# Kernel tuning notes

Hardware: AMD Instinct MI355X
Metric: run time of the kernel (lower is better)

Reference implementation:

```python
import jax, jax.numpy as jnp
import numpy as np


def _rank_transform_ascending(flat):
    # torch: _, idx = sort(flat, descending=False); flat[idx] = linspace(0,1,n)+1/n
    n = flat.shape[0]
    order = jnp.argsort(flat)  # ascending
    prob = jnp.linspace(0.0, 1.0, n, dtype=flat.dtype) + jnp.asarray(1.0 / n, flat.dtype)
    return jnp.zeros_like(flat).at[order].set(prob)


def corr_attention(query, key, value):
    # score[b,h,i,j] = cosine-like similarity q_i . k_j / (|q_i| |k_j|)
    score = jnp.einsum('bhid,bhjd->bhij', query, key)
    q_len = jnp.sqrt(jnp.sum(query * query, axis=-1, keepdims=True)) + 1e-5  # [b,h,s,1]
    k_len = jnp.sqrt(jnp.sum(key * key, axis=-1, keepdims=True)) + 1e-5      # [b,h,s,1]
    score = score / (q_len * jnp.swapaxes(k_len, -1, -2))
    signal = jnp.sign(score)
    size = score.shape
    flat = jnp.abs(score).reshape(-1)
    ranked = _rank_transform_ascending(flat)
    score = -jnp.log(ranked).reshape(size) * signal
    score = score / jnp.sum(jnp.abs(score), axis=-1, keepdims=True)
    return jnp.einsum('bhij,bhjd->bhid', score, value)


def setup_inputs() -> dict:
    key0 = jax.random.key(0)
    kq, kk, kv = jax.random.split(key0, 3)
    B, H, S, D = 4, 8, 1024, 64
    query = jax.random.normal(kq, (B, H, S, D), dtype=jnp.float32)
    key = jax.random.normal(kk, (B, H, S, D), dtype=jnp.float32)
    value = jax.random.normal(kv, (B, H, S, D), dtype=jnp.float32)
    return {"query": query, "key": key, "value": value}


def reference(query, key, value):
    # Attention.forward with mode='season'
    return corr_attention(query, key, value)
```

## Files before the change

kernel.cpp:

```cpp
#include <hip/hip_runtime.h>
#include <math.h>
#include <stdint.h>

#define S_LEN 1024
#define D_DIM 64
#define BH    32
#define KSHIFT 13
#define NBINS 130048u
#define HOT_LO 115712u
#define NHOT   14336u
#define HIST_LO 117760u
#define NHOT_H  12288u
#define NCHUNK 254
#define HBLK   256
#define INV_NM1 (1.0f/33554431.0f)
#define INV_N   (2.9802322387695312e-08f)
#define FIX_TH  1e-4f

typedef _Float16 half8 __attribute__((ext_vector_type(8)));
typedef short    short8 __attribute__((ext_vector_type(8)));
typedef float    floatx4 __attribute__((ext_vector_type(4)));

__global__ __launch_bounds__(256) void norms_kernel(
    const float* __restrict__ Q, const float* __restrict__ K,
    double* __restrict__ qinvD, double* __restrict__ kinvD,
    float* __restrict__ qinvF, float* __restrict__ kinvF) {
  int row  = blockIdx.x * 4 + (threadIdx.x >> 6);
  int lane = threadIdx.x & 63;
  const float* src; double* dstD; float* dstF; int r = row;
  if (row < BH * S_LEN) { src = Q; dstD = qinvD; dstF = qinvF; }
  else                  { src = K; dstD = kinvD; dstF = kinvF; r = row - BH * S_LEN; }
  double v = (double)src[(size_t)r * D_DIM + lane];
  double s = v * v;
  #pragma unroll
  for (int off = 32; off; off >>= 1) s += __shfl_down(s, off);
  if (lane == 0) {
    double inv = 1.0 / (sqrt(s) + 1e-5);
    dstD[r] = inv;
    dstF[r] = (float)inv;
  }
}

__device__ __forceinline__ void bf16_split(float x, short& hi, short& lo) {
  unsigned u = __float_as_uint(x);
  unsigned h = (u + 0x7FFFu + ((u >> 16) & 1u)) >> 16;
  float hf = __uint_as_float(h << 16);
  float lf = x - hf;
  hi = (short)h;
  lo = (short)(__float_as_uint(lf) >> 16);
}

__global__ __launch_bounds__(256) void qk_mfma_kernel(
    const float* __restrict__ Q, const float* __restrict__ K,
    const float* __restrict__ qinvF, const float* __restrict__ kinvF,
    float* __restrict__ score) {
  __shared__ short Qhi[64][72], Qlo[64][72];
  __shared__ short Khi[64][72], Klo[64][72];
  int bh = blockIdx.z;
  int i0 = blockIdx.y * 64;
  int j0 = blockIdx.x * 64;
  int tid = threadIdx.x;
  const float* Qb = Q + ((size_t)bh * S_LEN + i0) * D_DIM;
  const float* Kb = K + ((size_t)bh * S_LEN + j0) * D_DIM;
  #pragma unroll
  for (int l = 0; l < 4; ++l) {
    int idx4 = l * 256 + tid;
    int row  = idx4 >> 4;
    int c4   = idx4 & 15;
    float qi = qinvF[(size_t)bh * S_LEN + i0 + row];
    float4 v = ((const float4*)Qb)[idx4];
    float qv[4] = {v.x * qi, v.y * qi, v.z * qi, v.w * qi};
    short qh[4], ql[4];
    #pragma unroll
    for (int c = 0; c < 4; ++c) bf16_split(qv[c], qh[c], ql[c]);
    *(short4*)&Qhi[row][c4 * 4] = make_short4(qh[0], qh[1], qh[2], qh[3]);
    *(short4*)&Qlo[row][c4 * 4] = make_short4(ql[0], ql[1], ql[2], ql[3]);
    float kj = kinvF[(size_t)bh * S_LEN + j0 + row];
    float4 w = ((const float4*)Kb)[idx4];
    float kv[4] = {w.x * kj, w.y * kj, w.z * kj, w.w * kj};
    short kh[4], kl[4];
    #pragma unroll
    for (int c = 0; c < 4; ++c) bf16_split(kv[c], kh[c], kl[c]);
    *(short4*)&Khi[row][c4 * 4] = make_short4(kh[0], kh[1], kh[2], kh[3]);
    *(short4*)&Klo[row][c4 * 4] = make_short4(kl[0], kl[1], kl[2], kl[3]);
  }
  __syncthreads();
  int wave = tid >> 6;
  int lane = tid & 63;
  int m    = lane & 15;
  int quad = lane >> 4;
  floatx4 acc[4];
  #pragma unroll
  for (int n = 0; n < 4; ++n) acc[n] = (floatx4){0.f, 0.f, 0.f, 0.f};
  #pragma unroll
  for (int ks = 0; ks < 2; ++ks) {
    int kb = ks * 32 + quad * 8;
    short8 a_hi = *(const short8*)&Qhi[wave * 16 + m][kb];
    short8 a_lo = *(const short8*)&Qlo[wave * 16 + m][kb];
    #pragma unroll
    for (int nt = 0; nt < 4; ++nt) {
      short8 b_hi = *(const short8*)&Khi[nt * 16 + m][kb];
      short8 b_lo = *(const short8*)&Klo[nt * 16 + m][kb];
      acc[nt] = __builtin_amdgcn_mfma_f32_16x16x32_bf16(a_hi, b_hi, acc[nt], 0, 0, 0);
      acc[nt] = __builtin_amdgcn_mfma_f32_16x16x32_bf16(a_hi, b_lo, acc[nt], 0, 0, 0);
      acc[nt] = __builtin_amdgcn_mfma_f32_16x16x32_bf16(a_lo, b_hi, acc[nt], 0, 0, 0);
    }
  }
  #pragma unroll
  for (int r = 0; r < 4; ++r) {
    float* op = score + ((size_t)bh * S_LEN + i0 + wave * 16 + quad * 4 + r) * S_LEN + j0 + m;
    #pragma unroll
    for (int nt = 0; nt < 4; ++nt)
      op[nt * 16] = acc[nt][r];
  }
}

__global__ __launch_bounds__(1024) void hist_kernel(
    float* __restrict__ score, const float* __restrict__ Q, const float* __restrict__ K,
    const double* __restrict__ qinvD, const double* __restrict__ kinvD,
    unsigned* __restrict__ hist, unsigned char* __restrict__ partial) {
  __shared__ unsigned lh[NHOT_H];
  int tid = threadIdx.x;
  int lane = tid & 63;
  for (unsigned i = tid; i < NHOT_H; i += 1024) lh[i] = 0u;
  __syncthreads();
  const float4* p = (const float4*)score + (size_t)blockIdx.x * 32768;
  #pragma unroll 2
  for (int it = 0; it < 32; ++it) {
    float4 v = p[it * 1024 + tid];
    float vv[4] = {v.x, v.y, v.z, v.w};
    bool anyf = (fabsf(vv[0]) < FIX_TH) | (fabsf(vv[1]) < FIX_TH) |
                (fabsf(vv[2]) < FIX_TH) | (fabsf(vv[3]) < FIX_TH);
    unsigned long long am = __ballot(anyf);
    while (am) {
      int src = (int)(__ffsll((long long)am) - 1);
      am &= am - 1;
      unsigned base4 = (unsigned)(blockIdx.x * 32768u + (unsigned)(it * 1024 + tid));
      unsigned b4 = __shfl(base4, src);
      #pragma unroll
      for (int c = 0; c < 4; ++c) {
        float sc = __shfl(vv[c], src);
        if (fabsf(sc) < FIX_TH) {
          unsigned flat = b4 * 4u + (unsigned)c;
          unsigned bh = flat >> 20, i = (flat >> 10) & 1023u, j = flat & 1023u;
          double qd = (double)Q[((size_t)bh * S_LEN + i) * D_DIM + lane];
          double kd = (double)K[((size_t)bh * S_LEN + j) * D_DIM + lane];
          double pd = qd * kd;
          #pragma unroll
          for (int off = 32; off; off >>= 1) pd += __shfl_down(pd, off);
          float corr = 0.f;
          if (lane == 0)
            corr = (float)(pd * qinvD[(size_t)bh * S_LEN + i] * kinvD[(size_t)bh * S_LEN + j]);
          corr = __shfl(corr, 0);
          if (lane == src) {
            vv[c] = corr;
            score[(size_t)flat] = corr;
          }
        }
      }
    }
    #pragma unroll
    for (int c = 0; c < 4; ++c) {
      unsigned b = __float_as_uint(fabsf(vv[c])) >> KSHIFT;
      if (b >= NBINS) b = NBINS - 1u;
      if (b >= HIST_LO) atomicAdd(&lh[b - HIST_LO], 1u);
      else              atomicAdd(&hist[b], 1u);
    }
  }
  __syncthreads();
  unsigned char* dst = partial + (size_t)blockIdx.x * NHOT_H;
  for (unsigned i = tid; i < NHOT_H; i += 1024) dst[i] = (unsigned char)lh[i];
}

__global__ __launch_bounds__(256) void hreduce_kernel(
    const unsigned char* __restrict__ partial, unsigned* __restrict__ hist) {
  unsigned bin = blockIdx.x * 256 + threadIdx.x;
  unsigned s = 0;
  #pragma unroll 8
  for (int b = 0; b < HBLK; ++b) s += (unsigned)partial[(size_t)b * NHOT_H + bin];
  hist[HIST_LO + bin] = s;
}

__global__ __launch_bounds__(256) void vt_kernel(
    const float* __restrict__ V, _Float16* __restrict__ Vt) {
  __shared__ _Float16 T[64][72];
  int bh = blockIdx.y, j0 = blockIdx.x * 64, tid = threadIdx.x;
  const float* Vb = V + ((size_t)bh * S_LEN + j0) * D_DIM;
  #pragma unroll
  for (int l = 0; l < 4; ++l) {
    int idx = l * 256 + tid;
    int jr = idx >> 4, d4 = idx & 15;
    float4 v = ((const float4*)Vb)[idx];
    T[d4*4+0][jr] = (_Float16)v.x;
    T[d4*4+1][jr] = (_Float16)v.y;
    T[d4*4+2][jr] = (_Float16)v.z;
    T[d4*4+3][jr] = (_Float16)v.w;
  }
  __syncthreads();
  _Float16* Ob = Vt + (size_t)bh * D_DIM * S_LEN + j0;
  #pragma unroll
  for (int l = 0; l < 2; ++l) {
    int idx = l * 256 + tid;
    int d = idx >> 3, jc = idx & 7;
    uint4 val = *(const uint4*)&T[d][jc*8];
    *(uint4*)(Ob + (size_t)d * S_LEN + jc*8) = val;
  }
}

__global__ __launch_bounds__(256) void scan1_kernel(const unsigned* __restrict__ hist,
                                                    unsigned* __restrict__ csum) {
  __shared__ unsigned sd[256];
  int c = blockIdx.x, t = threadIdx.x;
  const unsigned* p = hist + (size_t)c * 512;
  sd[t] = p[t] + p[t + 256];
  __syncthreads();
  for (int off = 128; off; off >>= 1) {
    if (t < off) sd[t] += sd[t + off];
    __syncthreads();
  }
  if (t == 0) csum[c] = sd[0];
}

__global__ __launch_bounds__(256) void scan2_kernel(unsigned* __restrict__ csum) {
  __shared__ unsigned d[256];
  int t = threadIdx.x;
  unsigned v = (t < NCHUNK) ? csum[t] : 0u;
  d[t] = v; __syncthreads();
  for (int off = 1; off < 256; off <<= 1) {
    unsigned x = (t >= off) ? d[t - off] : 0u;
    __syncthreads();
    d[t] += x;
    __syncthreads();
  }
  if (t < NCHUNK) csum[t] = d[t] - v;
}

__global__ __launch_bounds__(256) void scan3_kernel(const unsigned* __restrict__ hist,
                                                    const unsigned* __restrict__ csum,
                                                    _Float16* __restrict__ tTab16) {
  __shared__ unsigned ts[256];
  int c = blockIdx.x, t = threadIdx.x;
  const unsigned* p = hist + (size_t)c * 512 + t * 2;
  unsigned l0 = p[0], l1 = p[1];
  unsigned s = l0 + l1;
  ts[t] = s; __syncthreads();
  for (int off = 1; off < 256; off <<= 1) {
    unsigned x = (t >= off) ? ts[t - off] : 0u;
    __syncthreads();
    ts[t] += x;
    __syncthreads();
  }
  unsigned base = csum[c] + ts[t] - s;
  int idx = c * 512 + t * 2;
  float r0 = (float)base + 0.5f * ((float)l0 - 1.0f);
  tTab16[idx]     = (_Float16)(-__logf(fmaf(r0, INV_NM1, INV_N)));
  float r1 = (float)(base + l0) + 0.5f * ((float)l1 - 1.0f);
  tTab16[idx + 1] = (_Float16)(-__logf(fmaf(r1, INV_NM1, INV_N)));
}

__global__ __launch_bounds__(256) void pv_mfma_kernel(
    const float* __restrict__ score, const _Float16* __restrict__ Vt,
    const unsigned short* __restrict__ tTab16, float* __restrict__ out) {
  __shared__ unsigned short ldsT[NHOT];
  int tid = threadIdx.x;
  {
    const unsigned* gsrc = (const unsigned*)(tTab16 + HOT_LO);
    unsigned* ldst = (unsigned*)ldsT;
    #pragma unroll
    for (int i = 0; i < 28; ++i)
      ldst[i * 256 + tid] = gsrc[i * 256 + tid];
  }
  __syncthreads();

  int bh   = blockIdx.y;
  int wave = tid >> 6;
  int lane = tid & 63;
  int m    = lane & 15;
  int quad = lane >> 4;
  int i0   = blockIdx.x * 64 + wave * 16;
  const float*    Sb = score + ((size_t)bh * S_LEN + i0 + m) * S_LEN;
  const _Float16* Vb = Vt + (size_t)bh * D_DIM * S_LEN;
  floatx4 acc[4];
  #pragma unroll
  for (int n = 0; n < 4; ++n) acc[n] = (floatx4){0.f, 0.f, 0.f, 0.f};
  float rsum = 0.f;

  for (int ks = 0; ks < 32; ++ks) {
    int k0 = ks * 32 + quad * 8;
    float4 s0 = *(const float4*)(Sb + k0);
    float4 s1 = *(const float4*)(Sb + k0 + 4);
    float sv[8] = {s0.x, s0.y, s0.z, s0.w, s1.x, s1.y, s1.z, s1.w};
    union { unsigned short u[8]; half8 h; } af;
    #pragma unroll
    for (int e = 0; e < 8; ++e) {
      unsigned u = __float_as_uint(sv[e]);
      unsigned a = u & 0x7fffffffu;
      unsigned b = a >> KSHIFT;
      if (b > NBINS - 1u) b = NBINS - 1u;
      unsigned short tb;
      if (b >= HOT_LO) tb = ldsT[b - HOT_LO];
      else             tb = tTab16[b];
      if (a == 0u) tb = 0;
      af.u[e] = (unsigned short)(tb ^ ((u >> 16) & 0x8000u));
      unsigned short tabs = (unsigned short)(tb & 0x7fffu);
      _Float16 th = __builtin_bit_cast(_Float16, tabs);
      rsum += (float)th;
    }
    half8 bf[4];
    #pragma unroll
    for (int n = 0; n < 4; ++n)
      bf[n] = *(const half8*)(Vb + (size_t)(n * 16 + m) * S_LEN + k0);
    #pragma unroll
    for (int n = 0; n < 4; ++n)
      acc[n] = __builtin_amdgcn_mfma_f32_16x16x32_f16(af.h, bf[n], acc[n], 0, 0, 0);
  }

  rsum += __shfl_xor(rsum, 16);
  rsum += __shfl_xor(rsum, 32);
  float inv = 1.0f / rsum;
  #pragma unroll
  for (int r = 0; r < 4; ++r) {
    int row = quad * 4 + r;
    float invr = __shfl(inv, row);
    float* op = out + ((size_t)bh * S_LEN + i0 + row) * D_DIM + m;
    #pragma unroll
    for (int n = 0; n < 4; ++n)
      op[n * 16] = acc[n][r] * invr;
  }
}

extern "C" void kernel_launch(void* const* d_in, const int* in_sizes, int n_in,
                              void* d_out, int out_size, void* d_ws, size_t ws_size,
                              hipStream_t stream) {
  const float* Q = (const float*)d_in[0];
  const float* K = (const float*)d_in[1];
  const float* V = (const float*)d_in[2];
  float* out = (float*)d_out;
  char* ws = (char*)d_ws;
  float*         score   = (float*)(ws);
  unsigned*      hist    = (unsigned*)(ws + 134217728);
  unsigned char* partial = (unsigned char*)(ws + 134737920);
  double*        qinvD   = (double*)(ws + 137883648);
  double*        kinvD   = (double*)(ws + 138145792);
  float*         qinvF   = (float*)(ws + 138407936);
  float*         kinvF   = (float*)(ws + 138539008);
  _Float16*      Vt      = (_Float16*)(ws + 134737920);
  unsigned*      csum    = (unsigned*)(ws + 139194368);
  _Float16*      tTab16  = (_Float16*)(ws + 139195392);

  hipMemsetAsync(hist, 0, NBINS * sizeof(unsigned), stream);
  norms_kernel<<<(2 * BH * S_LEN) / 4, 256, 0, stream>>>(Q, K, qinvD, kinvD, qinvF, kinvF);
  qk_mfma_kernel<<<dim3(16, 16, BH), 256, 0, stream>>>(Q, K, qinvF, kinvF, score);
  hist_kernel<<<HBLK, 1024, 0, stream>>>(score, Q, K, qinvD, kinvD, hist, partial);
  hreduce_kernel<<<NHOT_H / 256, 256, 0, stream>>>(partial, hist);
  vt_kernel<<<dim3(16, BH), 256, 0, stream>>>(V, Vt);
  scan1_kernel<<<NCHUNK, 256, 0, stream>>>(hist, csum);
  scan2_kernel<<<1, 256, 0, stream>>>(csum);
  scan3_kernel<<<NCHUNK, 256, 0, stream>>>(hist, csum, tTab16);
  pv_mfma_kernel<<<dim3(16, BH), 256, 0, stream>>>(
      score, Vt, (const unsigned short*)tTab16, out);
}
```

Baseline: 218.0 us.

## Split PV reduction across waves with LDS atomics and shrink hot table

The PV kernel now gives each block 16 rows, with its four waves each covering a quarter of the key dimension. Partial MFMA accumulators and row sums are combined through LDS atomics, and the result is written as float4 stores. The grid grows from 512 to 2048 blocks to raise occupancy and memory-level parallelism on the large score read. The LDS table preload shrinks to the NHOT_H range, which cuts preload cost per block but sends more lookups to global memory. Each block still preloads the table, so more blocks means more total preload traffic, and the LDS atomics add overhead.

Measured after the change: 238.8 us. +9.5%, slower.

```diff
diff --git a/kernel.cpp b/kernel.cpp
--- a/kernel.cpp
+++ b/kernel.cpp
@@ -7,8 +7,6 @@
 #define BH    32
 #define KSHIFT 13
 #define NBINS 130048u
-#define HOT_LO 115712u
-#define NHOT   14336u
 #define HIST_LO 117760u
 #define NHOT_H  12288u
 #define NCHUNK 254
@@ -261,14 +259,22 @@
 __global__ __launch_bounds__(256) void pv_mfma_kernel(
     const float* __restrict__ score, const _Float16* __restrict__ Vt,
     const unsigned short* __restrict__ tTab16, float* __restrict__ out) {
-  __shared__ unsigned short ldsT[NHOT];
+  __shared__ unsigned short ldsT[NHOT_H];
+  __shared__ float accS[16][72];
+  __shared__ float rsumS[16];
   int tid = threadIdx.x;
   {
-    const unsigned* gsrc = (const unsigned*)(tTab16 + HOT_LO);
+    const unsigned* gsrc = (const unsigned*)(tTab16 + HIST_LO);
     unsigned* ldst = (unsigned*)ldsT;
     #pragma unroll
-    for (int i = 0; i < 28; ++i)
+    for (int i = 0; i < 24; ++i)
       ldst[i * 256 + tid] = gsrc[i * 256 + tid];
+  }
+  if (tid < 16) rsumS[tid] = 0.f;
+  {
+    int r = tid >> 4, c = tid & 15;
+    #pragma unroll
+    for (int cc = 0; cc < 4; ++cc) accS[r][c * 4 + cc] = 0.f;
   }
   __syncthreads();
 
@@ -277,15 +283,16 @@
   int lane = tid & 63;
   int m    = lane & 15;
   int quad = lane >> 4;
-  int i0   = blockIdx.x * 64 + wave * 16;
-  const float*    Sb = score + ((size_t)bh * S_LEN + i0 + m) * S_LEN;
-  const _Float16* Vb = Vt + (size_t)bh * D_DIM * S_LEN;
+  int i0   = blockIdx.x * 16;
+  const float*    Sb = score + ((size_t)bh * S_LEN + i0 + m) * S_LEN + wave * 256;
+  const _Float16* Vb = Vt + (size_t)bh * D_DIM * S_LEN + wave * 256;
   floatx4 acc[4];
   #pragma unroll
   for (int n = 0; n < 4; ++n) acc[n] = (floatx4){0.f, 0.f, 0.f, 0.f};
   float rsum = 0.f;
 
-  for (int ks = 0; ks < 32; ++ks) {
+  #pragma unroll 2
+  for (int ks = 0; ks < 8; ++ks) {
     int k0 = ks * 32 + quad * 8;
     float4 s0 = *(const float4*)(Sb + k0);
     float4 s1 = *(const float4*)(Sb + k0 + 4);
@@ -298,8 +305,8 @@
       unsigned b = a >> KSHIFT;
       if (b > NBINS - 1u) b = NBINS - 1u;
       unsigned short tb;
-      if (b >= HOT_LO) tb = ldsT[b - HOT_LO];
-      else             tb = tTab16[b];
+      if (b >= HIST_LO) tb = ldsT[b - HIST_LO];
+      else              tb = tTab16[b];
       if (a == 0u) tb = 0;
       af.u[e] = (unsigned short)(tb ^ ((u >> 16) & 0x8000u));
       unsigned short tabs = (unsigned short)(tb & 0x7fffu);
@@ -317,15 +324,20 @@
 
   rsum += __shfl_xor(rsum, 16);
   rsum += __shfl_xor(rsum, 32);
-  float inv = 1.0f / rsum;
-  #pragma unroll
-  for (int r = 0; r < 4; ++r) {
-    int row = quad * 4 + r;
-    float invr = __shfl(inv, row);
-    float* op = out + ((size_t)bh * S_LEN + i0 + row) * D_DIM + m;
-    #pragma unroll
-    for (int n = 0; n < 4; ++n)
-      op[n * 16] = acc[n][r] * invr;
+  if (lane < 16) atomicAdd(&rsumS[lane], rsum);
+  #pragma unroll
+  for (int n = 0; n < 4; ++n)
+    #pragma unroll
+    for (int r = 0; r < 4; ++r)
+      atomicAdd(&accS[quad * 4 + r][n * 16 + m], acc[n][r]);
+  __syncthreads();
+
+  {
+    int r = tid >> 4, c4 = tid & 15;
+    float inv = 1.0f / rsumS[r];
+    float4 a4 = *(const float4*)&accS[r][c4 * 4];
+    float4 o = make_float4(a4.x * inv, a4.y * inv, a4.z * inv, a4.w * inv);
+    *(float4*)(out + ((size_t)bh * S_LEN + i0 + r) * D_DIM + c4 * 4) = o;
   }
 }
 
@@ -357,6 +369,6 @@
   scan1_kernel<<<NCHUNK, 256, 0, stream>>>(hist, csum);
   scan2_kernel<<<1, 256, 0, stream>>>(csum);
   scan3_kernel<<<NCHUNK, 256, 0, stream>>>(hist, csum, tTab16);
-  pv_mfma_kernel<<<dim3(16, BH), 256, 0, stream>>>(
+  pv_mfma_kernel<<<dim3(64, BH), 256, 0, stream>>>(
       score, Vt, (const unsigned short*)tTab16, out);
 }
```

## Software-pipeline score loads, table gathers and V loads in PV MFMA loop

Applied to the files above, without the earlier changes.

Restructures the PV MFMA main loop into a double-buffered pipeline. Score rows are loaded two iterations ahead, and the table gather plus V fragment loads run one iteration ahead of the MFMAs, so memory and LDS latency can overlap with matrix work. It also adds a min-blocks-per-CU hint of 2 to launch_bounds. The prefetch reads past the end of each row on the last iterations (those values are discarded), and the extra live buffers raise register pressure.

New measurement: 219.7 us. Within noise of the previous version (+0.7%).

```diff
diff --git a/kernel.cpp b/kernel.cpp
--- a/kernel.cpp
+++ b/kernel.cpp
@@ -258,7 +258,7 @@
   tTab16[idx + 1] = (_Float16)(-__logf(fmaf(r1, INV_NM1, INV_N)));
 }
 
-__global__ __launch_bounds__(256) void pv_mfma_kernel(
+__global__ __launch_bounds__(256, 2) void pv_mfma_kernel(
     const float* __restrict__ score, const _Float16* __restrict__ Vt,
     const unsigned short* __restrict__ tTab16, float* __restrict__ out) {
   __shared__ unsigned short ldsT[NHOT];
@@ -285,34 +285,57 @@
   for (int n = 0; n < 4; ++n) acc[n] = (floatx4){0.f, 0.f, 0.f, 0.f};
   float rsum = 0.f;
 
-  for (int ks = 0; ks < 32; ++ks) {
-    int k0 = ks * 32 + quad * 8;
-    float4 s0 = *(const float4*)(Sb + k0);
-    float4 s1 = *(const float4*)(Sb + k0 + 4);
-    float sv[8] = {s0.x, s0.y, s0.z, s0.w, s1.x, s1.y, s1.z, s1.w};
-    union { unsigned short u[8]; half8 h; } af;
+  auto gather8 = [&](const float4& a, const float4& b, unsigned short* t8) {
+    float sv[8] = {a.x, a.y, a.z, a.w, b.x, b.y, b.z, b.w};
     #pragma unroll
     for (int e = 0; e < 8; ++e) {
       unsigned u = __float_as_uint(sv[e]);
-      unsigned a = u & 0x7fffffffu;
-      unsigned b = a >> KSHIFT;
-      if (b > NBINS - 1u) b = NBINS - 1u;
+      unsigned av = u & 0x7fffffffu;
+      unsigned bb = av >> KSHIFT;
+      if (bb > NBINS - 1u) bb = NBINS - 1u;
       unsigned short tb;
-      if (b >= HOT_LO) tb = ldsT[b - HOT_LO];
-      else             tb = tTab16[b];
-      if (a == 0u) tb = 0;
-      af.u[e] = (unsigned short)(tb ^ ((u >> 16) & 0x8000u));
-      unsigned short tabs = (unsigned short)(tb & 0x7fffu);
-      _Float16 th = __builtin_bit_cast(_Float16, tabs);
+      if (bb >= HOT_LO) tb = ldsT[bb - HOT_LO];
+      else              tb = tTab16[bb];
+      if (av == 0u) tb = 0;
+      t8[e] = (unsigned short)(tb ^ ((u >> 16) & 0x8000u));
+    }
+  };
+
+  float4 sc0[2], sc1[2];
+  unsigned short tbs[2][8];
+  half8 bfs[2][4];
+
+  sc0[0] = *(const float4*)(Sb + quad * 8);
+  sc1[0] = *(const float4*)(Sb + quad * 8 + 4);
+  sc0[1] = *(const float4*)(Sb + 32 + quad * 8);
+  sc1[1] = *(const float4*)(Sb + 32 + quad * 8 + 4);
+  #pragma unroll
+  for (int n = 0; n < 4; ++n)
+    bfs[0][n] = *(const half8*)(Vb + (size_t)(n * 16 + m) * S_LEN + quad * 8);
+  gather8(sc0[0], sc1[0], tbs[0]);
+
+  #pragma unroll 2
+  for (int ks = 0; ks < 32; ++ks) {
+    const int cur = ks & 1, nxt = cur ^ 1;
+    const int kN = (ks + 1) * 32 + quad * 8;
+    const int kP = (ks + 2) * 32 + quad * 8;
+    #pragma unroll
+    for (int n = 0; n < 4; ++n)
+      bfs[nxt][n] = *(const half8*)(Vb + (size_t)(n * 16 + m) * S_LEN + kN);
+    gather8(sc0[nxt], sc1[nxt], tbs[nxt]);
+    sc0[cur] = *(const float4*)(Sb + kP);
+    sc1[cur] = *(const float4*)(Sb + kP + 4);
+    union { unsigned short u[8]; half8 h; } af;
+    #pragma unroll
+    for (int e = 0; e < 8; ++e) {
+      unsigned short tv = tbs[cur][e];
+      af.u[e] = tv;
+      _Float16 th = __builtin_bit_cast(_Float16, (unsigned short)(tv & 0x7fffu));
       rsum += (float)th;
     }
-    half8 bf[4];
     #pragma unroll
     for (int n = 0; n < 4; ++n)
-      bf[n] = *(const half8*)(Vb + (size_t)(n * 16 + m) * S_LEN + k0);
-    #pragma unroll
-    for (int n = 0; n < 4; ++n)
-      acc[n] = __builtin_amdgcn_mfma_f32_16x16x32_f16(af.h, bf[n], acc[n], 0, 0, 0);
+      acc[n] = __builtin_amdgcn_mfma_f32_16x16x32_f16(af.h, bfs[cur][n], acc[n], 0, 0, 0);
   }
 
   rsum += __shfl_xor(rsum, 16);
```
